# Kernel tuning notes

Hardware: AMD Instinct MI355X
Metric: run time of the kernel (lower is better)

## Reference

```python
import jax, jax.numpy as jnp
import numpy as np

N_NODES = 50000
N_EDGES = 800000
D_IN = 128
D_OUT = 128


def setup_inputs() -> dict:
    key = jax.random.key(0)
    k1, k2, k3, k4, k5 = jax.random.split(key, 5)
    x = jax.random.normal(k1, (N_NODES, D_IN), dtype=jnp.float32)
    edge_index = jax.random.randint(k2, (2, N_EDGES), 0, N_NODES, dtype=jnp.int64)
    # PyG SAGEConv params: lin_l (neighbors, with bias), lin_r (root, no bias)
    scale = 1.0 / np.sqrt(D_IN)
    W_l = jax.random.uniform(k3, (D_OUT, D_IN), dtype=jnp.float32, minval=-scale, maxval=scale)
    b_l = jax.random.uniform(k4, (D_OUT,), dtype=jnp.float32, minval=-scale, maxval=scale)
    W_r = jax.random.uniform(k5, (D_OUT, D_IN), dtype=jnp.float32, minval=-scale, maxval=scale)
    return {"x": x, "edge_index": edge_index, "W_l": W_l, "b_l": b_l, "W_r": W_r}


def reference(x, edge_index, W_l, b_l, W_r):
    src, dst = edge_index[0], edge_index[1]
    # mean aggregation of neighbor (source) features into destination nodes
    msg = x[src]  # [E, D_IN]
    agg_sum = jax.ops.segment_sum(msg, dst, num_segments=N_NODES)  # [N, D_IN]
    deg = jax.ops.segment_sum(jnp.ones((N_EDGES,), dtype=x.dtype), dst, num_segments=N_NODES)
    agg = agg_sum / jnp.maximum(deg, 1.0)[:, None]  # isolated nodes -> 0
    # out = lin_l(agg) + lin_r(x); ReLU from SAGE_NET wrapper (active=True)
    out = agg @ W_l.T + b_l + x @ W_r.T
    return jax.nn.relu(out)
```

## Files before the change

### kernel.cpp

```cpp
#include <hip/hip_runtime.h>
#include <hip/hip_bf16.h>

#define NNODES 50000
#define NEDGES 800000
#define DD 128
#define WPITCH 129
#define CAP 64
#define FILL_B 1563
#define XCV_B 6250
#define WB_B 64

typedef unsigned int u32;
typedef unsigned short u16;
typedef short bf16x8 __attribute__((ext_vector_type(8)));
typedef float f32x4 __attribute__((ext_vector_type(4)));
typedef float f32x2 __attribute__((ext_vector_type(2)));

#if defined(__has_builtin)
#if __has_builtin(__builtin_amdgcn_cvt_pk_f32_fp8)
#define HAVE_HW_FP8 1
#endif
#endif

union U4B8 {
    uint4 u;
    bf16x8 b;
};

__device__ __forceinline__ u32 f2b(float f) {
    u32 u = __float_as_uint(f);
    u32 rounding = 0x7fffu + ((u >> 16) & 1u);
    return (u + rounding) >> 16;
}

__device__ __forceinline__ u32 f2e4m3(float f) {
    u32 u = __float_as_uint(f);
    u32 s = (u >> 31) << 7;
    u32 mag = u & 0x7fffffffu;
    if (mag < 0x3c800000u) return s;
    u32 t = mag + 0x0007FFFFu + ((mag >> 20) & 1u);
    u32 e = (t >> 23) - 120u;
    u32 m = (t >> 20) & 7u;
    if (e > 15u || (e == 15u && m == 7u)) { e = 15u; m = 6u; }
    return s | (e << 3) | m;
}

__device__ __forceinline__ void fp8x4_acc(u32 v, float& a0, float& a1,
                                          float& a2, float& a3) {
#ifdef HAVE_HW_FP8
    f32x2 lo = __builtin_amdgcn_cvt_pk_f32_fp8((int)v, false);
    f32x2 hi = __builtin_amdgcn_cvt_pk_f32_fp8((int)v, true);
    a0 += lo.x;
    a1 += lo.y;
    a2 += hi.x;
    a3 += hi.y;
#else
#pragma unroll
    for (int b = 0; b < 4; ++b) {
        u32 byte = (v >> (8 * b)) & 0xffu;
        u32 f = ((byte >> 7) << 31) | ((((byte >> 3) & 15u) + 120u) << 23) |
                ((byte & 7u) << 20);
        float val = (byte & 0x78u) ? __uint_as_float(f) : 0.f;
        if (b == 0) a0 += val;
        else if (b == 1) a1 += val;
        else if (b == 2) a2 += val;
        else a3 += val;
    }
#endif
}

__global__ __launch_bounds__(256) void work_k(
    const int* __restrict__ ei, u32* __restrict__ deg,
    u16* __restrict__ slots16, const float* __restrict__ x,
    u32* __restrict__ xb, u32* __restrict__ xq,
    const float* __restrict__ Wl, const float* __restrict__ Wr,
    u32* __restrict__ wb) {
    const int b = blockIdx.x, tid = threadIdx.x;
    if (b < FILL_B) {
        u32 t = (u32)b * 256u + tid;
        if (t < (u32)(NEDGES / 2)) {
            uint2 s = ((const uint2*)ei)[t];
            uint2 d = ((const uint2*)(ei + NEDGES))[t];
            u32 p0 = atomicAdd(deg + d.x, 1u);
            u32 p1 = atomicAdd(deg + d.y, 1u);
            if (p0 < CAP) slots16[(size_t)d.x * CAP + p0] = (u16)s.x;
            if (p1 < CAP) slots16[(size_t)d.y * CAP + p1] = (u16)s.y;
        }
    } else if (b < FILL_B + XCV_B) {
        int i = (b - FILL_B) * 256 + tid;
        float4 v = ((const float4*)x)[i];
        uint2 o;
        o.x = f2b(v.x) | (f2b(v.y) << 16);
        o.y = f2b(v.z) | (f2b(v.w) << 16);
        ((uint2*)xb)[i] = o;
        xq[i] = f2e4m3(v.x) | (f2e4m3(v.y) << 8) | (f2e4m3(v.z) << 16) |
                (f2e4m3(v.w) << 24);
    } else {
        int idx = (b - FILL_B - XCV_B) * 256 + tid;
        int o = idx >> 7, c = idx & 127, k0 = 2 * c;
        const float* src = (k0 < DD) ? (Wl + o * DD + k0) : (Wr + o * DD + (k0 - DD));
        wb[idx] = f2b(src[0]) | (f2b(src[1]) << 16);
    }
}

__global__ __launch_bounds__(256) void gather_fp8_k(
    const u32* __restrict__ xq, const u16* __restrict__ slots16,
    const u32* __restrict__ deg, u32* __restrict__ aggb) {
    u32 gid = blockIdx.x * 256u + threadIdx.x;
    u32 node = gid >> 6;
    u32 lane = gid & 63u;
    if (node >= NNODES) return;
    u32 d = deg[node];
    u32 cnt = min(d, (u32)CAP);
    u32 sv = (lane < cnt) ? (u32)slots16[(size_t)node * CAP + lane] : 0u;
    const u32 half = lane >> 5;
    const u32 q = lane & 31u;
    float a0 = 0.f, a1 = 0.f, a2 = 0.f, a3 = 0.f;
    u32 j = 0;
    for (; j + 16 <= cnt; j += 16) {
        u32 v[8];
#pragma unroll
        for (int p = 0; p < 8; ++p) {
            u32 sA = __shfl(sv, (int)(j + 2 * p), 64);
            u32 sB = __shfl(sv, (int)(j + 2 * p + 1), 64);
            u32 s = half ? sB : sA;
            v[p] = xq[(size_t)s * 32 + q];
        }
#pragma unroll
        for (int p = 0; p < 8; ++p) fp8x4_acc(v[p], a0, a1, a2, a3);
    }
    for (; j + 2 <= cnt; j += 2) {
        u32 sA = __shfl(sv, (int)j, 64);
        u32 sB = __shfl(sv, (int)(j + 1), 64);
        u32 s = half ? sB : sA;
        fp8x4_acc(xq[(size_t)s * 32 + q], a0, a1, a2, a3);
    }
    if (j < cnt) {
        u32 sA = __shfl(sv, (int)j, 64);
        u32 v = xq[(size_t)sA * 32 + q];
        if (!half) fp8x4_acc(v, a0, a1, a2, a3);
    }
    a0 += __shfl_xor(a0, 32, 64);
    a1 += __shfl_xor(a1, 32, 64);
    a2 += __shfl_xor(a2, 32, 64);
    a3 += __shfl_xor(a3, 32, 64);
    if (lane < 32) {
        float inv = 1.0f / fmaxf((float)d, 1.0f);
        uint2 o;
        o.x = f2b(a0 * inv) | (f2b(a1 * inv) << 16);
        o.y = f2b(a2 * inv) | (f2b(a3 * inv) << 16);
        *(uint2*)&aggb[(size_t)node * 64 + q * 2] = o;
    }
}

__global__ __launch_bounds__(256) void mfma_fused_k(
    const u32* __restrict__ aggb, const u32* __restrict__ xb,
    const u32* __restrict__ wb, const float* __restrict__ bl,
    float* __restrict__ out) {
    __shared__ u32 w_lds[DD * WPITCH];
    __shared__ float sbias[DD];
    const int tid = threadIdx.x;
    for (int r = tid >> 5; r < DD; r += 8) {
        int c = (tid & 31) * 4;
        uint4 v = *(const uint4*)&wb[r * DD + c];
        *(uint4*)&w_lds[r * WPITCH + c] = v;
    }
    if (tid < DD) sbias[tid] = bl[tid];
    __syncthreads();

    const int wave = tid >> 6, lane = tid & 63;
    const int m = lane & 15, quad = lane >> 4;
    const int row0 = blockIdx.x * 128 + wave * 32;

    f32x4 acc[2][8];
#pragma unroll
    for (int t = 0; t < 2; ++t)
#pragma unroll
        for (int nt = 0; nt < 8; ++nt) acc[t][nt] = (f32x4){0.f, 0.f, 0.f, 0.f};

    for (int ks = 0; ks < 8; ++ks) {
        const u32* A = (ks < 4) ? aggb : xb;
        const int kc = (ks & 3) * 16 + quad * 4;
        U4B8 af[2];
#pragma unroll
        for (int t = 0; t < 2; ++t) {
            int r = row0 + t * 16 + m;
            r = r < NNODES ? r : NNODES - 1;
            af[t].u = *(const uint4*)&A[(size_t)r * 64 + kc];
        }
#pragma unroll
        for (int nt = 0; nt < 8; ++nt) {
            U4B8 bf;
            bf.u = *(const uint4*)&w_lds[(nt * 16 + m) * WPITCH + ks * 16 + quad * 4];
            acc[0][nt] = __builtin_amdgcn_mfma_f32_16x16x32_bf16(
                af[0].b, bf.b, acc[0][nt], 0, 0, 0);
            acc[1][nt] = __builtin_amdgcn_mfma_f32_16x16x32_bf16(
                af[1].b, bf.b, acc[1][nt], 0, 0, 0);
        }
    }
#pragma unroll
    for (int t = 0; t < 2; ++t) {
#pragma unroll
        for (int nt = 0; nt < 8; ++nt) {
            int col = nt * 16 + m;
            float b = sbias[col];
#pragma unroll
            for (int r = 0; r < 4; ++r) {
                int row = row0 + t * 16 + quad * 4 + r;
                if (row < NNODES)
                    out[(size_t)row * DD + col] = fmaxf(acc[t][nt][r] + b, 0.f);
            }
        }
    }
}

__global__ __launch_bounds__(256) void scatter_k(
    const float* __restrict__ x, const int* __restrict__ ei,
    float* __restrict__ agg, u32* __restrict__ deg) {
    u32 gid = blockIdx.x * 256u + threadIdx.x;
    u32 edge = gid >> 6;
    u32 lane = gid & 63u;
    if (edge >= NEDGES) return;
    int src = ei[edge];
    int dst = ei[NEDGES + edge];
    float2 v = ((const float2*)(x + (size_t)src * DD))[lane];
    float* p = agg + (size_t)dst * DD + lane * 2u;
    unsafeAtomicAdd(p, v.x);
    unsafeAtomicAdd(p + 1, v.y);
    if (lane == 0) atomicAdd(deg + dst, 1u);
}

__global__ __launch_bounds__(256) void mean_k(
    float* __restrict__ agg, const u32* __restrict__ deg) {
    u32 gid = blockIdx.x * 256u + threadIdx.x;
    u32 node = gid >> 6;
    u32 lane = gid & 63u;
    if (node >= NNODES) return;
    float inv = 1.0f / fmaxf((float)deg[node], 1.0f);
    float2* p = (float2*)(agg + (size_t)node * DD) + lane;
    float2 v = *p;
    *p = make_float2(v.x * inv, v.y * inv);
}

__global__ __launch_bounds__(256) void lin_l_k(
    float* __restrict__ agg,
    const float* __restrict__ Wl, const float* __restrict__ bl) {
    __shared__ u32 WT[DD * 65];
    __shared__ float rows[4 * DD];
    __shared__ float sbias[DD];
    const int tid = threadIdx.x;
    {
        u16* WTs = (u16*)WT;
        for (int i = tid; i < DD * DD; i += 256) {
            int o = i >> 7, k = i & 127;
            WTs[k * 130 + o] = (u16)f2b(Wl[i]);
        }
        if (tid < DD) sbias[tid] = bl[tid];
    }
    __syncthreads();
    const int h = tid & 63;
    const int nl = tid >> 6;
    for (int base = blockIdx.x * 4; base < NNODES; base += gridDim.x * 4) {
        ((float2*)rows)[tid] =
            ((const float2*)(agg + (size_t)(base + (tid >> 6)) * DD))[tid & 63];
        __syncthreads();
        float acc0 = sbias[2 * h], acc1 = sbias[2 * h + 1];
#pragma unroll
        for (int k = 0; k < DD; ++k) {
            float a = rows[nl * DD + k];
            u32 w2 = WT[k * 65 + h];
            acc0 = fmaf(a, __uint_as_float(w2 << 16), acc0);
            acc1 = fmaf(a, __uint_as_float(w2 & 0xffff0000u), acc1);
        }
        __syncthreads();
        ((float2*)(agg + (size_t)(base + nl) * DD))[h] = make_float2(acc0, acc1);
    }
}

__global__ __launch_bounds__(256) void lin_r_k(
    float* __restrict__ io, const float* __restrict__ x,
    const float* __restrict__ Wr) {
    __shared__ u32 WT[DD * 65];
    __shared__ float rows[4 * DD];
    const int tid = threadIdx.x;
    {
        u16* WTs = (u16*)WT;
        for (int i = tid; i < DD * DD; i += 256) {
            int o = i >> 7, k = i & 127;
            WTs[k * 130 + o] = (u16)f2b(Wr[i]);
        }
    }
    __syncthreads();
    const int h = tid & 63;
    const int nl = tid >> 6;
    for (int base = blockIdx.x * 4; base < NNODES; base += gridDim.x * 4) {
        ((float2*)rows)[tid] =
            ((const float2*)(x + (size_t)(base + (tid >> 6)) * DD))[tid & 63];
        __syncthreads();
        float2 t2 = ((const float2*)(io + (size_t)(base + nl) * DD))[h];
        float acc0 = t2.x, acc1 = t2.y;
#pragma unroll
        for (int k = 0; k < DD; ++k) {
            float a = rows[nl * DD + k];
            u32 w2 = WT[k * 65 + h];
            acc0 = fmaf(a, __uint_as_float(w2 << 16), acc0);
            acc1 = fmaf(a, __uint_as_float(w2 & 0xffff0000u), acc1);
        }
        acc0 = fmaxf(acc0, 0.f);
        acc1 = fmaxf(acc1, 0.f);
        __syncthreads();
        ((float2*)(io + (size_t)(base + nl) * DD))[h] = make_float2(acc0, acc1);
    }
}

extern "C" void kernel_launch(void* const* d_in, const int* in_sizes, int n_in,
                              void* d_out, int out_size, void* d_ws, size_t ws_size,
                              hipStream_t stream) {
    const float* x  = (const float*)d_in[0];
    const int*   ei = (const int*)d_in[1];
    const float* Wl = (const float*)d_in[2];
    const float* bl = (const float*)d_in[3];
    const float* Wr = (const float*)d_in[4];

    u32* deg     = (u32*)d_ws;
    u16* slots16 = (u16*)(deg + NNODES);
    u32* wb      = (u32*)d_ws + NNODES + (size_t)NNODES * (CAP / 2);
    u32* xb      = wb + 16384;
    u32* xq      = xb + (size_t)NNODES * 64;
    u32* aggb    = xq + (size_t)NNODES * 32;
    const size_t need =
        ((size_t)NNODES * (1 + CAP / 2 + 64 + 32 + 64) + 16384) * 4;

    if (ws_size >= need) {
        hipMemsetAsync(deg, 0, (size_t)NNODES * sizeof(u32), stream);
        work_k<<<FILL_B + XCV_B + WB_B, 256, 0, stream>>>(
            ei, deg, slots16, x, xb, xq, Wl, Wr, wb);
        gather_fp8_k<<<12500, 256, 0, stream>>>(xq, slots16, deg, aggb);
        mfma_fused_k<<<(NNODES + 127) / 128, 256, 0, stream>>>(
            aggb, xb, wb, bl, (float*)d_out);
    } else {
        float* agg = (float*)d_out;
        hipMemsetAsync(d_out, 0, (size_t)NNODES * DD * sizeof(float), stream);
        hipMemsetAsync(d_ws, 0, (size_t)NNODES * sizeof(u32), stream);
        scatter_k<<<(NEDGES * 64) / 256, 256, 0, stream>>>(x, ei, agg, deg);
        mean_k<<<(NNODES * 64 + 255) / 256, 256, 0, stream>>>(agg, deg);
        lin_l_k<<<1024, 256, 0, stream>>>(agg, Wl, bl);
        lin_r_k<<<1024, 256, 0, stream>>>(agg, x, Wr);
    }
}
```

Baseline: 170.4 us.

## Fuse neighbor gather with MFMA linear layers and partition CSR fill by destination

The fp8 neighbor gather and the bf16 MFMA linear stage are merged into one kernel of 512 threads. Each wave aggregates 16 nodes into LDS, then multiplies them against the W_l half and later the W_r half of the weights, which are staged in turn through a smaller LDS buffer. This removes the bf16 aggregate round-trip through global memory and one launch. Separately, the slot-fill pass now has 8 destination partitions, each scanning all edges but handling only its own range of destinations, which aims for atomic and write locality at the cost of reading the destination indices 8 times. The fused kernel runs only 391 blocks, so parallelism during the latency-bound gather drops, and the fill now launches far more blocks.

```diff
diff --git a/kernel.cpp b/kernel.cpp
--- a/kernel.cpp
+++ b/kernel.cpp
@@ -4,11 +4,13 @@
 #define NNODES 50000
 #define NEDGES 800000
 #define DD 128
-#define WPITCH 129
+#define NPART 8
+#define PSIZE 6250
 #define CAP 64
-#define FILL_B 1563
+#define FILL_B 25000
 #define XCV_B 6250
 #define WB_B 64
+#define WP2 68
 
 typedef unsigned int u32;
 typedef unsigned short u16;
@@ -77,14 +79,12 @@
     u32* __restrict__ wb) {
     const int b = blockIdx.x, tid = threadIdx.x;
     if (b < FILL_B) {
-        u32 t = (u32)b * 256u + tid;
-        if (t < (u32)(NEDGES / 2)) {
-            uint2 s = ((const uint2*)ei)[t];
-            uint2 d = ((const uint2*)(ei + NEDGES))[t];
-            u32 p0 = atomicAdd(deg + d.x, 1u);
-            u32 p1 = atomicAdd(deg + d.y, 1u);
-            if (p0 < CAP) slots16[(size_t)d.x * CAP + p0] = (u16)s.x;
-            if (p1 < CAP) slots16[(size_t)d.y * CAP + p1] = (u16)s.y;
+        u32 part = (u32)b & (NPART - 1);
+        u32 e = ((u32)b >> 3) * 256u + tid;
+        int dst = ei[NEDGES + e];
+        if ((u32)(dst - part * PSIZE) < (u32)PSIZE) {
+            u32 pos = atomicAdd(deg + dst, 1u);
+            if (pos < CAP) slots16[(size_t)dst * CAP + pos] = (u16)ei[e];
         }
     } else if (b < FILL_B + XCV_B) {
         int i = (b - FILL_B) * 256 + tid;
@@ -103,113 +103,136 @@
     }
 }
 
-__global__ __launch_bounds__(256) void gather_fp8_k(
+__global__ __launch_bounds__(512, 4) void sage_fused_k(
     const u32* __restrict__ xq, const u16* __restrict__ slots16,
-    const u32* __restrict__ deg, u32* __restrict__ aggb) {
-    u32 gid = blockIdx.x * 256u + threadIdx.x;
-    u32 node = gid >> 6;
-    u32 lane = gid & 63u;
-    if (node >= NNODES) return;
-    u32 d = deg[node];
-    u32 cnt = min(d, (u32)CAP);
-    u32 sv = (lane < cnt) ? (u32)slots16[(size_t)node * CAP + lane] : 0u;
+    const u32* __restrict__ deg, const u32* __restrict__ xb,
+    const u32* __restrict__ wb, const float* __restrict__ bl,
+    float* __restrict__ out) {
+    __shared__ u32 w2[DD * WP2];
+    __shared__ u32 agg_lds[128 * WP2];
+    __shared__ float sbias[DD];
+    const int tid = threadIdx.x;
+    const int row0 = blockIdx.x * 128;
+    const int wave = tid >> 6, lane = tid & 63;
+    const int m = lane & 15, quad = lane >> 4;
+
+    for (int r = tid >> 5; r < DD; r += 16) {
+        int c2 = (tid & 31) * 2;
+        *(uint2*)&w2[r * WP2 + c2] = *(const uint2*)&wb[r * DD + c2];
+    }
+    if (tid < DD) sbias[tid] = bl[tid];
+
+    uint4 af_x[4];
+    {
+        int r = row0 + wave * 16 + m;
+        r = r < NNODES ? r : NNODES - 1;
+        const u32* xrow = xb + (size_t)r * 64;
+#pragma unroll
+        for (int ks = 0; ks < 4; ++ks)
+            af_x[ks] = *(const uint4*)&xrow[ks * 16 + quad * 4];
+    }
+
     const u32 half = lane >> 5;
     const u32 q = lane & 31u;
-    float a0 = 0.f, a1 = 0.f, a2 = 0.f, a3 = 0.f;
-    u32 j = 0;
-    for (; j + 16 <= cnt; j += 16) {
-        u32 v[8];
-#pragma unroll
-        for (int p = 0; p < 8; ++p) {
-            u32 sA = __shfl(sv, (int)(j + 2 * p), 64);
-            u32 sB = __shfl(sv, (int)(j + 2 * p + 1), 64);
+    const u32 nbase = (u32)(row0 + wave * 16);
+    u32 d = (nbase < NNODES) ? deg[nbase] : 0u;
+    u32 sv = (nbase < NNODES) ? (u32)slots16[(size_t)nbase * CAP + lane] : 0u;
+    for (int i = 0; i < 16; ++i) {
+        u32 d_n = 0u, sv_n = 0u;
+        if (i < 15) {
+            u32 nn = nbase + (u32)i + 1u;
+            if (nn < NNODES) {
+                d_n = deg[nn];
+                sv_n = (u32)slots16[(size_t)nn * CAP + lane];
+            }
+        }
+        u32 cnt = min(d, (u32)CAP);
+        float a0 = 0.f, a1 = 0.f, a2 = 0.f, a3 = 0.f;
+        u32 j = 0;
+        for (; j + 16 <= cnt; j += 16) {
+            u32 v[8];
+#pragma unroll
+            for (int p = 0; p < 8; ++p) {
+                u32 sA = __shfl(sv, (int)(j + 2 * p), 64);
+                u32 sB = __shfl(sv, (int)(j + 2 * p + 1), 64);
+                u32 s = half ? sB : sA;
+                v[p] = xq[(size_t)s * 32 + q];
+            }
+#pragma unroll
+            for (int p = 0; p < 8; ++p) fp8x4_acc(v[p], a0, a1, a2, a3);
+        }
+        for (; j + 2 <= cnt; j += 2) {
+            u32 sA = __shfl(sv, (int)j, 64);
+            u32 sB = __shfl(sv, (int)(j + 1), 64);
             u32 s = half ? sB : sA;
-            v[p] = xq[(size_t)s * 32 + q];
-        }
-#pragma unroll
-        for (int p = 0; p < 8; ++p) fp8x4_acc(v[p], a0, a1, a2, a3);
-    }
-    for (; j + 2 <= cnt; j += 2) {
-        u32 sA = __shfl(sv, (int)j, 64);
-        u32 sB = __shfl(sv, (int)(j + 1), 64);
-        u32 s = half ? sB : sA;
-        fp8x4_acc(xq[(size_t)s * 32 + q], a0, a1, a2, a3);
-    }
-    if (j < cnt) {
-        u32 sA = __shfl(sv, (int)j, 64);
-        u32 v = xq[(size_t)sA * 32 + q];
-        if (!half) fp8x4_acc(v, a0, a1, a2, a3);
-    }
-    a0 += __shfl_xor(a0, 32, 64);
-    a1 += __shfl_xor(a1, 32, 64);
-    a2 += __shfl_xor(a2, 32, 64);
-    a3 += __shfl_xor(a3, 32, 64);
-    if (lane < 32) {
-        float inv = 1.0f / fmaxf((float)d, 1.0f);
-        uint2 o;
-        o.x = f2b(a0 * inv) | (f2b(a1 * inv) << 16);
-        o.y = f2b(a2 * inv) | (f2b(a3 * inv) << 16);
-        *(uint2*)&aggb[(size_t)node * 64 + q * 2] = o;
-    }
-}
-
-__global__ __launch_bounds__(256) void mfma_fused_k(
-    const u32* __restrict__ aggb, const u32* __restrict__ xb,
-    const u32* __restrict__ wb, const float* __restrict__ bl,
-    float* __restrict__ out) {
-    __shared__ u32 w_lds[DD * WPITCH];
-    __shared__ float sbias[DD];
-    const int tid = threadIdx.x;
-    for (int r = tid >> 5; r < DD; r += 8) {
-        int c = (tid & 31) * 4;
-        uint4 v = *(const uint4*)&wb[r * DD + c];
-        *(uint4*)&w_lds[r * WPITCH + c] = v;
-    }
-    if (tid < DD) sbias[tid] = bl[tid];
-    __syncthreads();
-
-    const int wave = tid >> 6, lane = tid & 63;
-    const int m = lane & 15, quad = lane >> 4;
-    const int row0 = blockIdx.x * 128 + wave * 32;
-
-    f32x4 acc[2][8];
-#pragma unroll
-    for (int t = 0; t < 2; ++t)
-#pragma unroll
-        for (int nt = 0; nt < 8; ++nt) acc[t][nt] = (f32x4){0.f, 0.f, 0.f, 0.f};
-
-    for (int ks = 0; ks < 8; ++ks) {
-        const u32* A = (ks < 4) ? aggb : xb;
-        const int kc = (ks & 3) * 16 + quad * 4;
-        U4B8 af[2];
-#pragma unroll
-        for (int t = 0; t < 2; ++t) {
-            int r = row0 + t * 16 + m;
-            r = r < NNODES ? r : NNODES - 1;
-            af[t].u = *(const uint4*)&A[(size_t)r * 64 + kc];
-        }
+            fp8x4_acc(xq[(size_t)s * 32 + q], a0, a1, a2, a3);
+        }
+        if (j < cnt) {
+            u32 sA = __shfl(sv, (int)j, 64);
+            u32 v = xq[(size_t)sA * 32 + q];
+            if (!half) fp8x4_acc(v, a0, a1, a2, a3);
+        }
+        a0 += __shfl_xor(a0, 32, 64);
+        a1 += __shfl_xor(a1, 32, 64);
+        a2 += __shfl_xor(a2, 32, 64);
+        a3 += __shfl_xor(a3, 32, 64);
+        if (lane < 32) {
+            float inv = 1.0f / fmaxf((float)d, 1.0f);
+            uint2 o;
+            o.x = f2b(a0 * inv) | (f2b(a1 * inv) << 16);
+            o.y = f2b(a2 * inv) | (f2b(a3 * inv) << 16);
+            *(uint2*)&agg_lds[(wave * 16 + i) * WP2 + q * 2] = o;
+        }
+        d = d_n;
+        sv = sv_n;
+    }
+    __syncthreads();
+
+    f32x4 acc[8];
+#pragma unroll
+    for (int nt = 0; nt < 8; ++nt) acc[nt] = (f32x4){0.f, 0.f, 0.f, 0.f};
+
+#pragma unroll
+    for (int ks = 0; ks < 4; ++ks) {
+        U4B8 af;
+        af.u = *(const uint4*)&agg_lds[(wave * 16 + m) * WP2 + ks * 16 + quad * 4];
 #pragma unroll
         for (int nt = 0; nt < 8; ++nt) {
             U4B8 bf;
-            bf.u = *(const uint4*)&w_lds[(nt * 16 + m) * WPITCH + ks * 16 + quad * 4];
-            acc[0][nt] = __builtin_amdgcn_mfma_f32_16x16x32_bf16(
-                af[0].b, bf.b, acc[0][nt], 0, 0, 0);
-            acc[1][nt] = __builtin_amdgcn_mfma_f32_16x16x32_bf16(
-                af[1].b, bf.b, acc[1][nt], 0, 0, 0);
-        }
-    }
-#pragma unroll
-    for (int t = 0; t < 2; ++t) {
+            bf.u = *(const uint4*)&w2[(nt * 16 + m) * WP2 + ks * 16 + quad * 4];
+            acc[nt] = __builtin_amdgcn_mfma_f32_16x16x32_bf16(af.b, bf.b,
+                                                              acc[nt], 0, 0, 0);
+        }
+    }
+    __syncthreads();
+    for (int r = tid >> 5; r < DD; r += 16) {
+        int c2 = (tid & 31) * 2;
+        *(uint2*)&w2[r * WP2 + c2] = *(const uint2*)&wb[r * DD + 64 + c2];
+    }
+    __syncthreads();
+
+#pragma unroll
+    for (int ks = 0; ks < 4; ++ks) {
+        U4B8 af;
+        af.u = af_x[ks];
 #pragma unroll
         for (int nt = 0; nt < 8; ++nt) {
-            int col = nt * 16 + m;
-            float b = sbias[col];
-#pragma unroll
-            for (int r = 0; r < 4; ++r) {
-                int row = row0 + t * 16 + quad * 4 + r;
-                if (row < NNODES)
-                    out[(size_t)row * DD + col] = fmaxf(acc[t][nt][r] + b, 0.f);
-            }
+            U4B8 bf;
+            bf.u = *(const uint4*)&w2[(nt * 16 + m) * WP2 + ks * 16 + quad * 4];
+            acc[nt] = __builtin_amdgcn_mfma_f32_16x16x32_bf16(af.b, bf.b,
+                                                              acc[nt], 0, 0, 0);
+        }
+    }
+
+#pragma unroll
+    for (int nt = 0; nt < 8; ++nt) {
+        int col = nt * 16 + m;
+        float b = sbias[col];
+#pragma unroll
+        for (int r_ = 0; r_ < 4; ++r_) {
+            int row = row0 + wave * 16 + quad * 4 + r_;
+            if (row < NNODES)
+                out[(size_t)row * DD + col] = fmaxf(acc[nt][r_] + b, 0.f);
         }
     }
 }
@@ -327,17 +350,15 @@
     u32* wb      = (u32*)d_ws + NNODES + (size_t)NNODES * (CAP / 2);
     u32* xb      = wb + 16384;
     u32* xq      = xb + (size_t)NNODES * 64;
-    u32* aggb    = xq + (size_t)NNODES * 32;
     const size_t need =
-        ((size_t)NNODES * (1 + CAP / 2 + 64 + 32 + 64) + 16384) * 4;
+        ((size_t)NNODES * (1 + CAP / 2 + 64 + 32) + 16384) * 4;
 
     if (ws_size >= need) {
         hipMemsetAsync(deg, 0, (size_t)NNODES * sizeof(u32), stream);
         work_k<<<FILL_B + XCV_B + WB_B, 256, 0, stream>>>(
             ei, deg, slots16, x, xb, xq, Wl, Wr, wb);
-        gather_fp8_k<<<12500, 256, 0, stream>>>(xq, slots16, deg, aggb);
-        mfma_fused_k<<<(NNODES + 127) / 128, 256, 0, stream>>>(
-            aggb, xb, wb, bl, (float*)d_out);
+        sage_fused_k<<<(NNODES + 127) / 128, 512, 0, stream>>>(
+            xq, slots16, deg, xb, wb, bl, (float*)d_out);
     } else {
         float* agg = (float*)d_out;
         hipMemsetAsync(d_out, 0, (size_t)NNODES * DD * sizeof(float), stream);
```

Measured after the change: 177.4 us. 4.1% more time.
